# Kernel tuning notes

Hardware: AMD Instinct MI355X
Metric: run time of the kernel (lower is better)

Reference implementation:

```python
import jax, jax.numpy as jnp
import numpy as np

N = 67108864  # 2**26 bytes per stream


def brev(x):
    """Reverse the 8 bits of each uint8 byte (same math as torch brev helper)."""
    x = x.astype(jnp.uint32)
    x = ((x & 0x55) << 1) | ((x >> 1) & 0x55)
    x = ((x & 0x33) << 2) | ((x >> 2) & 0x33)
    x = ((x & 0x0F) << 4) | ((x >> 4) & 0x0F)
    return x.astype(jnp.uint8)


def setup_inputs() -> dict:
    key = jax.random.key(0)
    k1, k2 = jax.random.split(key)
    a = jax.random.randint(k1, (N,), 0, 256, dtype=jnp.int32).astype(jnp.uint8)
    b = jax.random.randint(k2, (N,), 0, 256, dtype=jnp.int32).astype(jnp.uint8)
    return {"a": a, "b": b}


def _bs_add(a, b):
    """Bit-serial carry-propagate add: brev -> wrapping add -> global carry
    resolution via exclusive scan (cub_exclusive_scan equivalent) -> brev."""
    ar = brev(a)
    br = brev(b)
    c = ar + br                                   # uint8 wrapping add
    g = (c < ar).astype(jnp.uint8)                # carry generated (wrapped)
    p = (c == 255).astype(jnp.uint8)              # carry propagates (max)

    def op(l, r):
        gl, pl = l
        gr, pr = r
        return (gr | (pr & gl), pl & pr)

    gi, _ = jax.lax.associative_scan(op, (g.ravel(), p.ravel()))
    # exclusive scan: incoming carry for element i is carry-out of prefix [0, i)
    carry_in = jnp.concatenate([jnp.zeros((1,), jnp.uint8), gi[:-1]]).reshape(c.shape)
    res = (c + carry_in).astype(jnp.uint8)        # resolve carries (wrapping)
    return brev(res)


def reference(a, b):
    m_plus_c = _bs_add(a, b)          # BSAdd
    not_c = ~b                        # BSNot on original b
    return m_plus_c & not_c           # BSAnd
```

## Files before the change

### kernel.cpp

```cpp
#include <hip/hip_runtime.h>


#define BLK 256
#define EPT 16
#define TILE (BLK * EPT)

typedef int iv4 __attribute__((ext_vector_type(4)));

__device__ __forceinline__ unsigned gp_combine(unsigned l, unsigned r) {
    unsigned g = (r & 1u) | ((r >> 1) & l & 1u);
    unsigned p = (l >> 1) & (r >> 1) & 1u;
    return g | (p << 1);
}

__device__ __forceinline__ unsigned brev8(unsigned x) {
    return __brev(x) >> 24;
}

__global__ __launch_bounds__(BLK) void bss_onepass(const int* __restrict__ a,
                                                   const int* __restrict__ b,
                                                   int* __restrict__ out) {
    __shared__ unsigned sh_w[4];
    __shared__ unsigned s_cin;

    const int tid = threadIdx.x;
    const int lane = tid & 63;
    const int wid = tid >> 6;
    const long base0 = (long)blockIdx.x * TILE;
    const int base = (int)base0 + tid * EPT;

    if (wid == 0) {
        unsigned cb = 0u;
        long w = base0 - 64;
        for (;;) {
            long idx = w + lane;
            unsigned cc = 0u, gg = 0u;
            if (idx >= 0) {
                unsigned s = brev8((unsigned)a[idx]) + brev8((unsigned)b[idx]);
                cc = s & 0xFFu;
                gg = s >> 8;
            }
            unsigned long long m = __ballot(cc != 0xFFu);
            if (m) {
                int hi = 63 - __clzll(m);
                cb = (unsigned)__shfl((int)gg, hi, 64);
                break;
            }
            w -= 64;
        }
        if (lane == 0) s_cin = cb;
    }

    iv4 av[4], bv[4];
#pragma unroll
    for (int q = 0; q < 4; ++q) {
        av[q] = *reinterpret_cast<const iv4*>(a + base + q * 4);
        bv[q] = *reinterpret_cast<const iv4*>(b + base + q * 4);
    }
    const int* ae = reinterpret_cast<const int*>(av);
    const int* be = reinterpret_cast<const int*>(bv);

    unsigned c[EPT];
    unsigned G = 0u, P = 0u;
#pragma unroll
    for (int k = 0; k < EPT; ++k) {
        unsigned s = brev8((unsigned)ae[k]) + brev8((unsigned)be[k]);
        c[k] = s & 0xFFu;
        G |= (s >> 8) << k;
        P |= ((c[k] + 1u) >> 8) << k;
    }

    const unsigned GoP = G | P;
    const unsigned g_t = (G + GoP) >> EPT;
    const unsigned p_t = (P == 0xFFFFu) ? 1u : 0u;

    const unsigned long long Gw = __ballot(g_t != 0u);
    const unsigned long long Pw = __ballot(p_t != 0u);
    if (lane == 63) {
        unsigned long long Tw = Gw + (Gw | Pw);
        unsigned g_w = (unsigned)(Tw < Gw);
        unsigned p_w = (Pw == ~0ull) ? 1u : 0u;
        sh_w[wid] = g_w | (p_w << 1);
    }
    __syncthreads();

    unsigned pre = 2u;
#pragma unroll
    for (int w = 0; w < 3; ++w)
        if (w < wid) pre = gp_combine(pre, sh_w[w]);
    const unsigned cb = s_cin;
    const unsigned cw = (pre & 1u) | (((pre >> 1) & 1u) & cb);

    const unsigned long long Sw = Gw + (Gw | Pw) + (unsigned long long)cw;
    const unsigned c_t = (unsigned)(((Pw ^ Sw) >> lane) & 1ull);

    const unsigned Cm = P ^ (G + GoP + c_t);

    iv4 o[4];
    int* of = reinterpret_cast<int*>(o);
#pragma unroll
    for (int k = 0; k < EPT; ++k) {
        unsigned res = (c[k] + ((Cm >> k) & 1u)) & 0xFFu;
        of[k] = (int)(brev8(res) & (~(unsigned)be[k] & 0xFFu));
    }
#pragma unroll
    for (int q = 0; q < 4; ++q)
        *reinterpret_cast<iv4*>(out + base + q * 4) = o[q];
}

extern "C" void kernel_launch(void* const* d_in, const int* in_sizes, int n_in,
                              void* d_out, int out_size, void* d_ws, size_t ws_size,
                              hipStream_t stream) {
    const int* a = (const int*)d_in[0];
    const int* b = (const int*)d_in[1];
    int* out = (int*)d_out;
    const int n = in_sizes[0];
    const int nb = n / TILE;

    bss_onepass<<<nb, BLK, 0, stream>>>(a, b, out);
}
```

Before: 155.7 us.

## Double elements per thread to 32 and byte-pack intermediates in registers

Raises each thread's element count from 16 to 32, so each block covers twice the data and half as many blocks run the backward carry-lookback loop and block-level combine. Intermediate sums and the b values are packed four bytes per 32-bit register to keep register use in check, and the per-thread generate/propagate mask arithmetic moves to 64-bit to capture the carry-out of 32 lanes. This adds shift/mask work per element and means fewer resident waves, plus 32 loads per input in flight per thread.

```diff
diff --git a/kernel.cpp b/kernel.cpp
--- a/kernel.cpp
+++ b/kernel.cpp
@@ -2,7 +2,7 @@
 
 
 #define BLK 256
-#define EPT 16
+#define EPT 32
 #define TILE (BLK * EPT)
 
 typedef int iv4 __attribute__((ext_vector_type(4)));
@@ -51,28 +51,31 @@
         if (lane == 0) s_cin = cb;
     }
 
-    iv4 av[4], bv[4];
-#pragma unroll
-    for (int q = 0; q < 4; ++q) {
-        av[q] = *reinterpret_cast<const iv4*>(a + base + q * 4);
-        bv[q] = *reinterpret_cast<const iv4*>(b + base + q * 4);
-    }
-    const int* ae = reinterpret_cast<const int*>(av);
-    const int* be = reinterpret_cast<const int*>(bv);
-
-    unsigned c[EPT];
+    unsigned cpack[8], bpack[8];
     unsigned G = 0u, P = 0u;
 #pragma unroll
-    for (int k = 0; k < EPT; ++k) {
-        unsigned s = brev8((unsigned)ae[k]) + brev8((unsigned)be[k]);
-        c[k] = s & 0xFFu;
-        G |= (s >> 8) << k;
-        P |= ((c[k] + 1u) >> 8) << k;
+    for (int q = 0; q < 8; ++q) {
+        iv4 av = *reinterpret_cast<const iv4*>(a + base + q * 4);
+        iv4 bv = *reinterpret_cast<const iv4*>(b + base + q * 4);
+        unsigned cp = 0u, bp = 0u;
+#pragma unroll
+        for (int j = 0; j < 4; ++j) {
+            unsigned s = brev8((unsigned)av[j]) + brev8((unsigned)bv[j]);
+            unsigned cc = s & 0xFFu;
+            cp |= cc << (8 * j);
+            bp |= ((unsigned)bv[j] & 0xFFu) << (8 * j);
+            const int k = q * 4 + j;
+            G |= (s >> 8) << k;
+            P |= ((cc + 1u) >> 8) << k;
+        }
+        cpack[q] = cp;
+        bpack[q] = bp;
     }
 
     const unsigned GoP = G | P;
-    const unsigned g_t = (G + GoP) >> EPT;
-    const unsigned p_t = (P == 0xFFFFu) ? 1u : 0u;
+    const unsigned long long S0 = (unsigned long long)G + GoP;
+    const unsigned g_t = (unsigned)(S0 >> 32);
+    const unsigned p_t = (P == 0xFFFFFFFFu) ? 1u : 0u;
 
     const unsigned long long Gw = __ballot(g_t != 0u);
     const unsigned long long Pw = __ballot(p_t != 0u);
@@ -94,18 +97,19 @@
     const unsigned long long Sw = Gw + (Gw | Pw) + (unsigned long long)cw;
     const unsigned c_t = (unsigned)(((Pw ^ Sw) >> lane) & 1ull);
 
-    const unsigned Cm = P ^ (G + GoP + c_t);
+    const unsigned Cm = P ^ (unsigned)((unsigned long long)G + GoP + c_t);
 
-    iv4 o[4];
-    int* of = reinterpret_cast<int*>(o);
 #pragma unroll
-    for (int k = 0; k < EPT; ++k) {
-        unsigned res = (c[k] + ((Cm >> k) & 1u)) & 0xFFu;
-        of[k] = (int)(brev8(res) & (~(unsigned)be[k] & 0xFFu));
+    for (int q = 0; q < 8; ++q) {
+        iv4 o;
+#pragma unroll
+        for (int j = 0; j < 4; ++j) {
+            const int k = q * 4 + j;
+            unsigned res = (((cpack[q] >> (8 * j)) & 0xFFu) + ((Cm >> k) & 1u)) & 0xFFu;
+            o[j] = (int)(brev8(res) & (~(bpack[q] >> (8 * j)) & 0xFFu));
+        }
+        *reinterpret_cast<iv4*>(out + base + q * 4) = o;
     }
-#pragma unroll
-    for (int q = 0; q < 4; ++q)
-        *reinterpret_cast<iv4*>(out + base + q * 4) = o[q];
 }
 
 extern "C" void kernel_launch(void* const* d_in, const int* in_sizes, int n_in,
```

New measurement: 199.2 us. 1.28x slower.

## Resolve carry-in per wavefront instead of per block, removing shared-memory sync

Applied to the files above, without the earlier changes.

Each 64-lane wavefront now owns an independent 1024-element tile and finds its own incoming carry with a backward ballot search, instead of one wave per block searching while the others wait. This drops the shared-memory exchange of per-wave generate/propagate flags and the block-wide barrier. In exchange, every wave runs the lookback loop and issues the extra global reads, so the number of lookback reads rises fourfold, though they mostly hit cache.

```diff
diff --git a/kernel.cpp b/kernel.cpp
--- a/kernel.cpp
+++ b/kernel.cpp
@@ -3,34 +3,35 @@
 
 #define BLK 256
 #define EPT 16
-#define TILE (BLK * EPT)
+#define WTILE (64 * EPT)
 
 typedef int iv4 __attribute__((ext_vector_type(4)));
-
-__device__ __forceinline__ unsigned gp_combine(unsigned l, unsigned r) {
-    unsigned g = (r & 1u) | ((r >> 1) & l & 1u);
-    unsigned p = (l >> 1) & (r >> 1) & 1u;
-    return g | (p << 1);
-}
 
 __device__ __forceinline__ unsigned brev8(unsigned x) {
     return __brev(x) >> 24;
 }
 
-__global__ __launch_bounds__(BLK) void bss_onepass(const int* __restrict__ a,
-                                                   const int* __restrict__ b,
-                                                   int* __restrict__ out) {
-    __shared__ unsigned sh_w[4];
-    __shared__ unsigned s_cin;
-
+__global__ __launch_bounds__(BLK) void bss_wave(const int* __restrict__ a,
+                                                const int* __restrict__ b,
+                                                int* __restrict__ out) {
     const int tid = threadIdx.x;
     const int lane = tid & 63;
     const int wid = tid >> 6;
-    const long base0 = (long)blockIdx.x * TILE;
-    const int base = (int)base0 + tid * EPT;
+    const long gw = (long)blockIdx.x * (BLK / 64) + wid;
+    const long base0 = gw * WTILE;
+    const int base = (int)base0 + lane * EPT;
 
-    if (wid == 0) {
-        unsigned cb = 0u;
+    iv4 av[4], bv[4];
+#pragma unroll
+    for (int q = 0; q < 4; ++q) {
+        av[q] = *reinterpret_cast<const iv4*>(a + base + q * 4);
+        bv[q] = *reinterpret_cast<const iv4*>(b + base + q * 4);
+    }
+    const int* ae = reinterpret_cast<const int*>(av);
+    const int* be = reinterpret_cast<const int*>(bv);
+
+    unsigned cb = 0u;
+    {
         long w = base0 - 64;
         for (;;) {
             long idx = w + lane;
@@ -48,17 +49,7 @@
             }
             w -= 64;
         }
-        if (lane == 0) s_cin = cb;
     }
-
-    iv4 av[4], bv[4];
-#pragma unroll
-    for (int q = 0; q < 4; ++q) {
-        av[q] = *reinterpret_cast<const iv4*>(a + base + q * 4);
-        bv[q] = *reinterpret_cast<const iv4*>(b + base + q * 4);
-    }
-    const int* ae = reinterpret_cast<const int*>(av);
-    const int* be = reinterpret_cast<const int*>(bv);
 
     unsigned c[EPT];
     unsigned G = 0u, P = 0u;
@@ -76,22 +67,7 @@
 
     const unsigned long long Gw = __ballot(g_t != 0u);
     const unsigned long long Pw = __ballot(p_t != 0u);
-    if (lane == 63) {
-        unsigned long long Tw = Gw + (Gw | Pw);
-        unsigned g_w = (unsigned)(Tw < Gw);
-        unsigned p_w = (Pw == ~0ull) ? 1u : 0u;
-        sh_w[wid] = g_w | (p_w << 1);
-    }
-    __syncthreads();
-
-    unsigned pre = 2u;
-#pragma unroll
-    for (int w = 0; w < 3; ++w)
-        if (w < wid) pre = gp_combine(pre, sh_w[w]);
-    const unsigned cb = s_cin;
-    const unsigned cw = (pre & 1u) | (((pre >> 1) & 1u) & cb);
-
-    const unsigned long long Sw = Gw + (Gw | Pw) + (unsigned long long)cw;
+    const unsigned long long Sw = Gw + (Gw | Pw) + (unsigned long long)cb;
     const unsigned c_t = (unsigned)(((Pw ^ Sw) >> lane) & 1ull);
 
     const unsigned Cm = P ^ (G + GoP + c_t);
@@ -115,7 +91,7 @@
     const int* b = (const int*)d_in[1];
     int* out = (int*)d_out;
     const int n = in_sizes[0];
-    const int nb = n / TILE;
+    const int nblk = n / (WTILE * (BLK / 64));
 
-    bss_onepass<<<nb, BLK, 0, stream>>>(a, b, out);
+    bss_wave<<<nblk, BLK, 0, stream>>>(a, b, out);
 }
```

After: 152.2 us. 1.02x faster.
